# Kernel optimization log

Measured on AMD Instinct MI355X. Metric: run time of the kernel, lower is better.

Reference implementation:

```python
import jax, jax.numpy as jnp
import numpy as np

BN_EPS = 1e-5

def _bn(h, gamma, beta, mean, var):
    # inference-mode BatchNorm1d
    return (h - mean) * jax.lax.rsqrt(var + BN_EPS) * gamma + beta


def setup_inputs() -> dict:
    key = jax.random.key(0)
    ks = jax.random.split(key, 16)
    N, E, D_in, D, L = 100000, 640000, 256, 128, 3
    s = 0.05
    return {
        "x": jax.random.normal(ks[0], (N, D_in), jnp.float32),
        "edge_index": jax.random.randint(ks[1], (2, E), 0, N, jnp.int32),
        "W_in": jax.random.normal(ks[2], (D_in, D), jnp.float32) * s,
        "b_in": jax.random.normal(ks[3], (D,), jnp.float32) * s,
        "bn_in_gamma": jax.random.uniform(ks[4], (D,), jnp.float32, 0.5, 1.5),
        "bn_in_beta": jax.random.normal(ks[5], (D,), jnp.float32) * s,
        "bn_in_mean": jax.random.normal(ks[6], (D,), jnp.float32) * s,
        "bn_in_var": jax.random.uniform(ks[7], (D,), jnp.float32, 0.5, 1.5),
        "Wl": jax.random.normal(ks[8], (L, D, D), jnp.float32) * s,
        "bl": jax.random.normal(ks[9], (L, D), jnp.float32) * s,
        "Wr": jax.random.normal(ks[10], (L, D, D), jnp.float32) * s,
        "bn_gamma": jax.random.uniform(ks[11], (L, D), jnp.float32, 0.5, 1.5),
        "bn_beta": jax.random.normal(ks[12], (L, D), jnp.float32) * s,
        "bn_mean": jax.random.normal(ks[13], (L, D), jnp.float32) * s,
        "bn_var": jax.random.uniform(ks[14], (L, D), jnp.float32, 0.5, 1.5),
    }


def reference(x, edge_index, W_in, b_in, bn_in_gamma, bn_in_beta, bn_in_mean,
              bn_in_var, Wl, bl, Wr, bn_gamma, bn_beta, bn_mean, bn_var):
    N = x.shape[0]
    src, dst = edge_index[0], edge_index[1]
    # in-degree (clamped to 1 so isolated nodes aggregate to 0, matching PyG mean)
    deg = jax.ops.segment_sum(jnp.ones_like(dst, jnp.float32), dst, num_segments=N)
    deg = jnp.maximum(deg, 1.0)[:, None]  # [N, 1]

    # input projection + BN + ReLU (dropout = identity in eval)
    h = jax.nn.relu(_bn(x @ W_in + b_in, bn_in_gamma, bn_in_beta, bn_in_mean, bn_in_var))

    L = Wl.shape[0]
    for l in range(L):
        # SAGEConv(mean): lin_l(mean_j h_j) + lin_r(h_i)
        agg = jax.ops.segment_sum(h[src], dst, num_segments=N) / deg  # [N, D]
        h_new = agg @ Wl[l] + bl[l] + h @ Wr[l]
        h_new = jax.nn.relu(_bn(h_new, bn_gamma[l], bn_beta[l], bn_mean[l], bn_var[l]))
        h = h + h_new  # residual
    return h
```

## Files before the change

### kernel.cpp

```cpp
#include <hip/hip_runtime.h>

#define BN_EPS 1e-5f

typedef __bf16 bf16x8 __attribute__((ext_vector_type(8)));
typedef float f32x4 __attribute__((ext_vector_type(4)));
typedef unsigned int uint;
typedef unsigned short ushort;

__device__ __forceinline__ ushort f2bf(float f) {
  union { float f; uint u; } v; v.f = f;
  uint r = v.u + 0x7FFF + ((v.u >> 16) & 1);
  return (ushort)(r >> 16);
}
__device__ __forceinline__ float bf2f_lo(uint u) {
  union { uint i; float f; } v; v.i = u << 16; return v.f;
}
__device__ __forceinline__ float bf2f_hi(uint u) {
  union { uint i; float f; } v; v.i = u & 0xffff0000u; return v.f;
}
__device__ __forceinline__ uint pack2(float a, float b) {
  return (uint)f2bf(a) | ((uint)f2bf(b) << 16);
}


__global__ void hist_kernel(const int* __restrict__ dst, int* __restrict__ cnt, int E) {
  int e = blockIdx.x * 256 + threadIdx.x;
  if (e < E) atomicAdd(&cnt[dst[e]], 1);
}

__device__ __forceinline__ int block_exscan256(int v, int tid, int* ws4) {
  __syncthreads();
  int lane = tid & 63, w = tid >> 6;
  int x = v;
  #pragma unroll
  for (int off = 1; off < 64; off <<= 1) {
    int y = __shfl_up(x, off, 64);
    if (lane >= off) x += y;
  }
  if (lane == 63) ws4[w] = x;
  __syncthreads();
  if (tid == 0) {
    int s = 0;
    for (int i = 0; i < 4; ++i) { int t = ws4[i]; ws4[i] = s; s += t; }
  }
  __syncthreads();
  return ws4[w] + x - v;
}

__global__ void blocksum_kernel(const int* __restrict__ cnt, int* __restrict__ bsum, int N) {
  __shared__ int ws4[4];
  int tid = threadIdx.x;
  int i = blockIdx.x * 256 + tid;
  int v = (i < N) ? cnt[i] : 0;
  #pragma unroll
  for (int off = 32; off > 0; off >>= 1) v += __shfl_down(v, off, 64);
  if ((tid & 63) == 0) ws4[tid >> 6] = v;
  __syncthreads();
  if (tid == 0) bsum[blockIdx.x] = ws4[0] + ws4[1] + ws4[2] + ws4[3];
}

__global__ void scanbsum_kernel(const int* __restrict__ bsum, int* __restrict__ boff,
                                int NB, int* __restrict__ rowptr, int N, int E) {
  __shared__ int ws4[4];
  __shared__ int tot;
  int tid = threadIdx.x;
  int carry = 0;
  for (int base = 0; base < NB; base += 256) {
    int i = base + tid;
    int v = (i < NB) ? bsum[i] : 0;
    int ex = block_exscan256(v, tid, ws4);
    if (i < NB) boff[i] = carry + ex;
    if (tid == 255) tot = ex + v;
    __syncthreads();
    carry += tot;
  }
  if (tid == 0) rowptr[N] = E;
}

__global__ void writerowptr_kernel(const int* __restrict__ cnt, const int* __restrict__ boff,
                                   int* __restrict__ rowptr, int N) {
  __shared__ int ws4[4];
  int tid = threadIdx.x;
  int i = blockIdx.x * 256 + tid;
  int v = (i < N) ? cnt[i] : 0;
  int ex = block_exscan256(v, tid, ws4);
  if (i < N) rowptr[i] = boff[blockIdx.x] + ex;
}

__global__ void fill_kernel(const int* __restrict__ src, const int* __restrict__ dst,
                            const int* __restrict__ rowptr, int* __restrict__ cur,
                            int* __restrict__ col, int E) {
  int e = blockIdx.x * 256 + threadIdx.x;
  if (e < E) {
    int d = dst[e];
    int p = rowptr[d] + atomicAdd(&cur[d], 1);
    col[p] = src[e];
  }
}


__global__ void prep_weights_fm(const float* __restrict__ W_in, const float* __restrict__ Wl,
                                const float* __restrict__ Wr, ushort* __restrict__ Bfm) {
  int p = blockIdx.x * 256 + threadIdx.x;
  int mat = p >> 12;
  int rem = p & 4095;
  int half = rem >> 11;
  int rem2 = rem & 2047;
  int nt = rem2 >> 8, kt2 = (rem2 >> 6) & 3, lane = rem2 & 63;
  int n = nt * 16 + (lane & 15);
  int k0 = (half * 4 + kt2) * 32 + (lane >> 4) * 8;
  ushort tmp[8];
  #pragma unroll
  for (int j = 0; j < 8; ++j) {
    int k = k0 + j;
    float v;
    if (mat == 0) v = W_in[k * 128 + n];
    else {
      int l = mat - 1;
      v = (k < 128) ? Wl[l * 16384 + k * 128 + n] : Wr[l * 16384 + (k - 128) * 128 + n];
    }
    tmp[j] = f2bf(v);
  }
  *(uint4*)&Bfm[(size_t)p * 8] = *(const uint4*)tmp;
}


__global__ void agg_kernel(const int* __restrict__ rowptr, const int* __restrict__ col,
                           const ushort* __restrict__ h, ushort* __restrict__ agg, int N) {
  int node = blockIdx.x * 8 + (threadIdx.x >> 5);
  if (node >= N) return;
  int lane = threadIdx.x & 31;
  const ushort* hp = h + lane * 4;
  int beg = rowptr[node], end = rowptr[node + 1];
  int deg = end - beg;
  float di = 1.0f / (float)(deg > 0 ? deg : 1);
  float a0 = 0.f, a1 = 0.f, a2 = 0.f, a3 = 0.f;
  int e = beg;
  for (; e + 3 < end; e += 4) {
    uint2 v0 = *(const uint2*)(hp + (size_t)col[e] * 128);
    uint2 v1 = *(const uint2*)(hp + (size_t)col[e + 1] * 128);
    uint2 v2 = *(const uint2*)(hp + (size_t)col[e + 2] * 128);
    uint2 v3 = *(const uint2*)(hp + (size_t)col[e + 3] * 128);
    a0 += (bf2f_lo(v0.x) + bf2f_lo(v1.x)) + (bf2f_lo(v2.x) + bf2f_lo(v3.x));
    a1 += (bf2f_hi(v0.x) + bf2f_hi(v1.x)) + (bf2f_hi(v2.x) + bf2f_hi(v3.x));
    a2 += (bf2f_lo(v0.y) + bf2f_lo(v1.y)) + (bf2f_lo(v2.y) + bf2f_lo(v3.y));
    a3 += (bf2f_hi(v0.y) + bf2f_hi(v1.y)) + (bf2f_hi(v2.y) + bf2f_hi(v3.y));
  }
  for (; e < end; ++e) {
    uint2 v0 = *(const uint2*)(hp + (size_t)col[e] * 128);
    a0 += bf2f_lo(v0.x); a1 += bf2f_hi(v0.x);
    a2 += bf2f_lo(v0.y); a3 += bf2f_hi(v0.y);
  }
  uint2 o;
  o.x = pack2(a0 * di, a1 * di);
  o.y = pack2(a2 * di, a3 * di);
  *(uint2*)(agg + (size_t)node * 128 + lane * 4) = o;
}


template<bool F32OUT>
__global__ __launch_bounds__(256, 4)
void gemm_layer(const ushort* __restrict__ A0, const ushort* __restrict__ A1,
                const ushort* __restrict__ Bfm, const float* __restrict__ bias,
                const float* __restrict__ gamma, const float* __restrict__ beta,
                const float* __restrict__ mean, const float* __restrict__ var,
                const ushort* __restrict__ residual, void* __restrict__ out, int N) {
  __shared__ float Cb_all[4 * 16 * 68];
  int tid = threadIdx.x, wave = tid >> 6, lane = tid & 63;
  int wm = wave >> 1, wn = wave & 1, quad = lane >> 4, l16 = lane & 15;
  int m0 = blockIdx.x * 64;

  int rowm[2];
  #pragma unroll
  for (int mt = 0; mt < 2; ++mt) {
    int r = m0 + wm * 32 + mt * 16 + l16;
    rowm[mt] = r < N ? r : N - 1;
  }

  uint4 a_buf[2][2], b_buf[2][4];
  #pragma unroll
  for (int mt = 0; mt < 2; ++mt)
    a_buf[0][mt] = *(const uint4*)(A0 + (size_t)rowm[mt] * 128 + quad * 8);
  {
    const ushort* bp = Bfm + (size_t)(wn * 4 * 256 + lane) * 8;
    #pragma unroll
    for (int nt = 0; nt < 4; ++nt)
      b_buf[0][nt] = *(const uint4*)(bp + nt * 2048);
  }

  f32x4 acc[2][4] = {};

  #pragma unroll
  for (int kt = 0; kt < 8; ++kt) {
    if (kt < 7) {
      int k1 = kt + 1;
      const ushort* bse = (k1 < 4) ? A0 : A1;
      int ko = (k1 & 3) * 32 + quad * 8;
      #pragma unroll
      for (int mt = 0; mt < 2; ++mt)
        a_buf[k1 & 1][mt] = *(const uint4*)(bse + (size_t)rowm[mt] * 128 + ko);
      const ushort* bp = Bfm + ((size_t)(k1 >> 2) * 16384 +
                                (size_t)((wn * 4) * 256 + (k1 & 3) * 64 + lane) * 8);
      #pragma unroll
      for (int nt = 0; nt < 4; ++nt)
        b_buf[k1 & 1][nt] = *(const uint4*)(bp + nt * 2048);
    }
    __builtin_amdgcn_sched_barrier(0);
    #pragma unroll
    for (int mt = 0; mt < 2; ++mt) {
      bf16x8 af = __builtin_bit_cast(bf16x8, a_buf[kt & 1][mt]);
      #pragma unroll
      for (int nt = 0; nt < 4; ++nt)
        acc[mt][nt] = __builtin_amdgcn_mfma_f32_16x16x32_bf16(
            af, __builtin_bit_cast(bf16x8, b_buf[kt & 1][nt]), acc[mt][nt], 0, 0, 0);
    }
  }

  #pragma unroll
  for (int nt = 0; nt < 4; ++nt) {
    int c = wn * 64 + nt * 16 + l16;
    float sc = gamma[c] * rsqrtf(var[c] + BN_EPS);
    float sh = beta[c] - mean[c] * sc;
    float bi = bias[c];
    #pragma unroll
    for (int mt = 0; mt < 2; ++mt)
      #pragma unroll
      for (int r = 0; r < 4; ++r)
        acc[mt][nt][r] = fmaxf((acc[mt][nt][r] + bi) * sc + sh, 0.f);
  }

  float* Cb = Cb_all + wave * (16 * 68);
  #pragma unroll
  for (int mt = 0; mt < 2; ++mt) {
    #pragma unroll
    for (int nt = 0; nt < 4; ++nt)
      #pragma unroll
      for (int r = 0; r < 4; ++r)
        Cb[(quad * 4 + r) * 68 + nt * 16 + l16] = acc[mt][nt][r];
    #pragma unroll
    for (int i = 0; i < 4; ++i) {
      int idx = i * 64 + lane, rowl = idx >> 4, seg = idx & 15;
      int grow = m0 + wm * 32 + mt * 16 + rowl;
      if (grow < N) {
        float4 vv = *(float4*)&Cb[rowl * 68 + seg * 4];
        uint2 rv = *(const uint2*)(residual + (size_t)grow * 128 + wn * 64 + seg * 4);
        vv.x += bf2f_lo(rv.x); vv.y += bf2f_hi(rv.x);
        vv.z += bf2f_lo(rv.y); vv.w += bf2f_hi(rv.y);
        if (F32OUT) {
          *(float4*)((float*)out + (size_t)grow * 128 + wn * 64 + seg * 4) = vv;
        } else {
          uint2 o;
          o.x = pack2(vv.x, vv.y); o.y = pack2(vv.z, vv.w);
          *(uint2*)((ushort*)out + (size_t)grow * 128 + wn * 64 + seg * 4) = o;
        }
      }
    }
  }
}


__global__ __launch_bounds__(256, 4)
void gemm_in(const float* __restrict__ X, const ushort* __restrict__ Bfm,
             const float* __restrict__ bias,
             const float* __restrict__ gamma, const float* __restrict__ beta,
             const float* __restrict__ mean, const float* __restrict__ var,
             ushort* __restrict__ out, int N) {
  __shared__ float Cb_all[4 * 16 * 68];
  int tid = threadIdx.x, wave = tid >> 6, lane = tid & 63;
  int wm = wave >> 1, wn = wave & 1, quad = lane >> 4, l16 = lane & 15;
  int m0 = blockIdx.x * 64;

  int rowm[2];
  #pragma unroll
  for (int mt = 0; mt < 2; ++mt) {
    int r = m0 + wm * 32 + mt * 16 + l16;
    rowm[mt] = r < N ? r : N - 1;
  }

  float4 f_buf[2][2][2];
  uint4 b_buf[2][4];
  #pragma unroll
  for (int mt = 0; mt < 2; ++mt) {
    const float* p = X + (size_t)rowm[mt] * 256 + quad * 8;
    f_buf[0][mt][0] = *(const float4*)p;
    f_buf[0][mt][1] = *(const float4*)(p + 4);
  }
  {
    const ushort* bp = Bfm + (size_t)(wn * 4 * 256 + lane) * 8;
    #pragma unroll
    for (int nt = 0; nt < 4; ++nt)
      b_buf[0][nt] = *(const uint4*)(bp + nt * 2048);
  }

  f32x4 acc[2][4] = {};

  #pragma unroll
  for (int kt = 0; kt < 8; ++kt) {
    if (kt < 7) {
      int k1 = kt + 1;
      int ko = k1 * 32 + quad * 8;
      #pragma unroll
      for (int mt = 0; mt < 2; ++mt) {
        const float* p = X + (size_t)rowm[mt] * 256 + ko;
        f_buf[k1 & 1][mt][0] = *(const float4*)p;
        f_buf[k1 & 1][mt][1] = *(const float4*)(p + 4);
      }
      const ushort* bp = Bfm + ((size_t)(k1 >> 2) * 16384 +
                                (size_t)((wn * 4) * 256 + (k1 & 3) * 64 + lane) * 8);
      #pragma unroll
      for (int nt = 0; nt < 4; ++nt)
        b_buf[k1 & 1][nt] = *(const uint4*)(bp + nt * 2048);
    }
    __builtin_amdgcn_sched_barrier(0);
    #pragma unroll
    for (int mt = 0; mt < 2; ++mt) {
      float4 lo = f_buf[kt & 1][mt][0], hi = f_buf[kt & 1][mt][1];
      uint4 av;
      av.x = pack2(lo.x, lo.y); av.y = pack2(lo.z, lo.w);
      av.z = pack2(hi.x, hi.y); av.w = pack2(hi.z, hi.w);
      bf16x8 af = __builtin_bit_cast(bf16x8, av);
      #pragma unroll
      for (int nt = 0; nt < 4; ++nt)
        acc[mt][nt] = __builtin_amdgcn_mfma_f32_16x16x32_bf16(
            af, __builtin_bit_cast(bf16x8, b_buf[kt & 1][nt]), acc[mt][nt], 0, 0, 0);
    }
  }

  #pragma unroll
  for (int nt = 0; nt < 4; ++nt) {
    int c = wn * 64 + nt * 16 + l16;
    float sc = gamma[c] * rsqrtf(var[c] + BN_EPS);
    float sh = beta[c] - mean[c] * sc;
    float bi = bias[c];
    #pragma unroll
    for (int mt = 0; mt < 2; ++mt)
      #pragma unroll
      for (int r = 0; r < 4; ++r)
        acc[mt][nt][r] = fmaxf((acc[mt][nt][r] + bi) * sc + sh, 0.f);
  }

  float* Cb = Cb_all + wave * (16 * 68);
  #pragma unroll
  for (int mt = 0; mt < 2; ++mt) {
    #pragma unroll
    for (int nt = 0; nt < 4; ++nt)
      #pragma unroll
      for (int r = 0; r < 4; ++r)
        Cb[(quad * 4 + r) * 68 + nt * 16 + l16] = acc[mt][nt][r];
    #pragma unroll
    for (int i = 0; i < 4; ++i) {
      int idx = i * 64 + lane, rowl = idx >> 4, seg = idx & 15;
      int grow = m0 + wm * 32 + mt * 16 + rowl;
      if (grow < N) {
        float4 vv = *(float4*)&Cb[rowl * 68 + seg * 4];
        uint2 o;
        o.x = pack2(vv.x, vv.y); o.y = pack2(vv.z, vv.w);
        *(uint2*)(out + (size_t)grow * 128 + wn * 64 + seg * 4) = o;
      }
    }
  }
}


extern "C" void kernel_launch(void* const* d_in, const int* in_sizes, int n_in,
                              void* d_out, int out_size, void* d_ws, size_t ws_size,
                              hipStream_t stream) {
  const float* x      = (const float*)d_in[0];
  const int*   eidx   = (const int*)d_in[1];
  const float* W_in   = (const float*)d_in[2];
  const float* b_in   = (const float*)d_in[3];
  const float* bng_in = (const float*)d_in[4];
  const float* bnb_in = (const float*)d_in[5];
  const float* bnm_in = (const float*)d_in[6];
  const float* bnv_in = (const float*)d_in[7];
  const float* Wl     = (const float*)d_in[8];
  const float* bl     = (const float*)d_in[9];
  const float* Wr     = (const float*)d_in[10];
  const float* bng    = (const float*)d_in[11];
  const float* bnb    = (const float*)d_in[12];
  const float* bnm    = (const float*)d_in[13];
  const float* bnv    = (const float*)d_in[14];

  const int N = in_sizes[0] / 256;
  const int E = in_sizes[1] / 2;
  const int NB = (N + 255) / 256;
  const int* src = eidx;
  const int* dst = eidx + E;

  char* ws = (char*)d_ws;
  size_t off = 0;
  auto alloc = [&](size_t bytes) {
    void* p = ws + off;
    off = (off + bytes + 255) & ~(size_t)255;
    return p;
  };
  int* cnt      = (int*)alloc((size_t)N * 4);
  int* rowptr   = (int*)alloc((size_t)(N + 1) * 4);
  int* bsum     = (int*)alloc((size_t)NB * 4);
  int* boff     = (int*)alloc((size_t)NB * 4);
  int* col      = (int*)alloc((size_t)E * 4);
  ushort* Bfm   = (ushort*)alloc(4 * 32768 * 2);
  ushort* hA    = (ushort*)alloc((size_t)N * 128 * 2);
  ushort* hB    = (ushort*)alloc((size_t)N * 128 * 2);
  ushort* agg   = (ushort*)alloc((size_t)N * 128 * 2);
  (void)ws_size; (void)n_in; (void)out_size;

  const int EB = (E + 255) / 256;
  const int GB = (N + 63) / 64;

  hipMemsetAsync(cnt, 0, (size_t)N * 4, stream);
  hist_kernel<<<EB, 256, 0, stream>>>(dst, cnt, E);
  blocksum_kernel<<<NB, 256, 0, stream>>>(cnt, bsum, N);
  scanbsum_kernel<<<1, 256, 0, stream>>>(bsum, boff, NB, rowptr, N, E);
  writerowptr_kernel<<<NB, 256, 0, stream>>>(cnt, boff, rowptr, N);
  hipMemsetAsync(cnt, 0, (size_t)N * 4, stream);
  fill_kernel<<<EB, 256, 0, stream>>>(src, dst, rowptr, cnt, col, E);

  prep_weights_fm<<<64, 256, 0, stream>>>(W_in, Wl, Wr, Bfm);

  gemm_in<<<GB, 256, 0, stream>>>(x, Bfm, b_in, bng_in, bnb_in, bnm_in, bnv_in, hA, N);

  ushort* hbuf[2] = { hA, hB };
  for (int l = 0; l < 3; ++l) {
    const ushort* h_in = hbuf[l & 1];
    agg_kernel<<<(N + 7) / 8, 256, 0, stream>>>(rowptr, col, h_in, agg, N);
    const ushort* BfmL = Bfm + (size_t)(l + 1) * 32768;
    const float* biasL = bl + l * 128;
    if (l < 2) {
      gemm_layer<false><<<GB, 256, 0, stream>>>(agg, h_in, BfmL, biasL,
          bng + l * 128, bnb + l * 128, bnm + l * 128, bnv + l * 128,
          h_in, (void*)hbuf[(l + 1) & 1], N);
    } else {
      gemm_layer<true><<<GB, 256, 0, stream>>>(agg, h_in, BfmL, biasL,
          bng + l * 128, bnb + l * 128, bnm + l * 128, bnv + l * 128,
          h_in, d_out, N);
    }
  }
}
```

Measured before the change: 457.4 us.

## Fuse neighbor aggregation into layer GEMM and replace CSR scan with atomic reservation

```diff
diff --git a/kernel.cpp b/kernel.cpp
--- a/kernel.cpp
+++ b/kernel.cpp
@@ -28,147 +28,117 @@
   if (e < E) atomicAdd(&cnt[dst[e]], 1);
 }
 
-__device__ __forceinline__ int block_exscan256(int v, int tid, int* ws4) {
-  __syncthreads();
-  int lane = tid & 63, w = tid >> 6;
+__global__ void reserve_prep_kernel(const int* __restrict__ cnt, int* __restrict__ rowbeg,
+                                    int* __restrict__ cursor,
+                                    const float* __restrict__ W_in, const float* __restrict__ Wl,
+                                    const float* __restrict__ Wr, ushort* __restrict__ Bfm,
+                                    int NB, int N) {
+  int tid = threadIdx.x;
+  int b = blockIdx.x;
+  if (b >= NB) {
+    int p = (b - NB) * 256 + tid;
+    int mat = p >> 12;
+    int rem = p & 4095;
+    int half = rem >> 11;
+    int rem2 = rem & 2047;
+    int nt = rem2 >> 8, kt2 = (rem2 >> 6) & 3, lane = rem2 & 63;
+    int n = nt * 16 + (lane & 15);
+    int k0 = (half * 4 + kt2) * 32 + (lane >> 4) * 8;
+    ushort tmp[8];
+    #pragma unroll
+    for (int j = 0; j < 8; ++j) {
+      int k = k0 + j;
+      float v;
+      if (mat == 0) v = W_in[k * 128 + n];
+      else {
+        int l = mat - 1;
+        v = (k < 128) ? Wl[l * 16384 + k * 128 + n] : Wr[l * 16384 + (k - 128) * 128 + n];
+      }
+      tmp[j] = f2bf(v);
+    }
+    *(uint4*)&Bfm[(size_t)p * 8] = *(const uint4*)tmp;
+    return;
+  }
+  int i = b * 256 + tid;
+  int v = (i < N) ? cnt[i] : 0;
+  int lane = tid & 63;
   int x = v;
   #pragma unroll
   for (int off = 1; off < 64; off <<= 1) {
     int y = __shfl_up(x, off, 64);
     if (lane >= off) x += y;
   }
-  if (lane == 63) ws4[w] = x;
-  __syncthreads();
-  if (tid == 0) {
-    int s = 0;
-    for (int i = 0; i < 4; ++i) { int t = ws4[i]; ws4[i] = s; s += t; }
-  }
-  __syncthreads();
-  return ws4[w] + x - v;
-}
-
-__global__ void blocksum_kernel(const int* __restrict__ cnt, int* __restrict__ bsum, int N) {
-  __shared__ int ws4[4];
-  int tid = threadIdx.x;
-  int i = blockIdx.x * 256 + tid;
-  int v = (i < N) ? cnt[i] : 0;
-  #pragma unroll
-  for (int off = 32; off > 0; off >>= 1) v += __shfl_down(v, off, 64);
-  if ((tid & 63) == 0) ws4[tid >> 6] = v;
-  __syncthreads();
-  if (tid == 0) bsum[blockIdx.x] = ws4[0] + ws4[1] + ws4[2] + ws4[3];
-}
-
-__global__ void scanbsum_kernel(const int* __restrict__ bsum, int* __restrict__ boff,
-                                int NB, int* __restrict__ rowptr, int N, int E) {
-  __shared__ int ws4[4];
-  __shared__ int tot;
-  int tid = threadIdx.x;
-  int carry = 0;
-  for (int base = 0; base < NB; base += 256) {
-    int i = base + tid;
-    int v = (i < NB) ? bsum[i] : 0;
-    int ex = block_exscan256(v, tid, ws4);
-    if (i < NB) boff[i] = carry + ex;
-    if (tid == 255) tot = ex + v;
-    __syncthreads();
-    carry += tot;
-  }
-  if (tid == 0) rowptr[N] = E;
-}
-
-__global__ void writerowptr_kernel(const int* __restrict__ cnt, const int* __restrict__ boff,
-                                   int* __restrict__ rowptr, int N) {
-  __shared__ int ws4[4];
-  int tid = threadIdx.x;
-  int i = blockIdx.x * 256 + tid;
-  int v = (i < N) ? cnt[i] : 0;
-  int ex = block_exscan256(v, tid, ws4);
-  if (i < N) rowptr[i] = boff[blockIdx.x] + ex;
+  int ret = 0;
+  if (lane == 63) ret = atomicAdd(cursor, x);
+  int base = __shfl(ret, 63);
+  if (i < N) rowbeg[i] = base + x - v;
 }
 
 __global__ void fill_kernel(const int* __restrict__ src, const int* __restrict__ dst,
-                            const int* __restrict__ rowptr, int* __restrict__ cur,
+                            const int* __restrict__ rowbeg, int* __restrict__ cur,
                             int* __restrict__ col, int E) {
   int e = blockIdx.x * 256 + threadIdx.x;
   if (e < E) {
     int d = dst[e];
-    int p = rowptr[d] + atomicAdd(&cur[d], 1);
+    int p = rowbeg[d] + atomicAdd(&cur[d], 1);
     col[p] = src[e];
   }
-}
-
-
-__global__ void prep_weights_fm(const float* __restrict__ W_in, const float* __restrict__ Wl,
-                                const float* __restrict__ Wr, ushort* __restrict__ Bfm) {
-  int p = blockIdx.x * 256 + threadIdx.x;
-  int mat = p >> 12;
-  int rem = p & 4095;
-  int half = rem >> 11;
-  int rem2 = rem & 2047;
-  int nt = rem2 >> 8, kt2 = (rem2 >> 6) & 3, lane = rem2 & 63;
-  int n = nt * 16 + (lane & 15);
-  int k0 = (half * 4 + kt2) * 32 + (lane >> 4) * 8;
-  ushort tmp[8];
-  #pragma unroll
-  for (int j = 0; j < 8; ++j) {
-    int k = k0 + j;
-    float v;
-    if (mat == 0) v = W_in[k * 128 + n];
-    else {
-      int l = mat - 1;
-      v = (k < 128) ? Wl[l * 16384 + k * 128 + n] : Wr[l * 16384 + (k - 128) * 128 + n];
-    }
-    tmp[j] = f2bf(v);
-  }
-  *(uint4*)&Bfm[(size_t)p * 8] = *(const uint4*)tmp;
-}
-
-
-__global__ void agg_kernel(const int* __restrict__ rowptr, const int* __restrict__ col,
-                           const ushort* __restrict__ h, ushort* __restrict__ agg, int N) {
-  int node = blockIdx.x * 8 + (threadIdx.x >> 5);
-  if (node >= N) return;
-  int lane = threadIdx.x & 31;
-  const ushort* hp = h + lane * 4;
-  int beg = rowptr[node], end = rowptr[node + 1];
-  int deg = end - beg;
-  float di = 1.0f / (float)(deg > 0 ? deg : 1);
-  float a0 = 0.f, a1 = 0.f, a2 = 0.f, a3 = 0.f;
-  int e = beg;
-  for (; e + 3 < end; e += 4) {
-    uint2 v0 = *(const uint2*)(hp + (size_t)col[e] * 128);
-    uint2 v1 = *(const uint2*)(hp + (size_t)col[e + 1] * 128);
-    uint2 v2 = *(const uint2*)(hp + (size_t)col[e + 2] * 128);
-    uint2 v3 = *(const uint2*)(hp + (size_t)col[e + 3] * 128);
-    a0 += (bf2f_lo(v0.x) + bf2f_lo(v1.x)) + (bf2f_lo(v2.x) + bf2f_lo(v3.x));
-    a1 += (bf2f_hi(v0.x) + bf2f_hi(v1.x)) + (bf2f_hi(v2.x) + bf2f_hi(v3.x));
-    a2 += (bf2f_lo(v0.y) + bf2f_lo(v1.y)) + (bf2f_lo(v2.y) + bf2f_lo(v3.y));
-    a3 += (bf2f_hi(v0.y) + bf2f_hi(v1.y)) + (bf2f_hi(v2.y) + bf2f_hi(v3.y));
-  }
-  for (; e < end; ++e) {
-    uint2 v0 = *(const uint2*)(hp + (size_t)col[e] * 128);
-    a0 += bf2f_lo(v0.x); a1 += bf2f_hi(v0.x);
-    a2 += bf2f_lo(v0.y); a3 += bf2f_hi(v0.y);
-  }
-  uint2 o;
-  o.x = pack2(a0 * di, a1 * di);
-  o.y = pack2(a2 * di, a3 * di);
-  *(uint2*)(agg + (size_t)node * 128 + lane * 4) = o;
 }
 
 
 template<bool F32OUT>
 __global__ __launch_bounds__(256, 4)
-void gemm_layer(const ushort* __restrict__ A0, const ushort* __restrict__ A1,
+void gemm_fused(const int* __restrict__ rowbeg, const int* __restrict__ deg,
+                const int* __restrict__ col, const ushort* __restrict__ h,
                 const ushort* __restrict__ Bfm, const float* __restrict__ bias,
                 const float* __restrict__ gamma, const float* __restrict__ beta,
                 const float* __restrict__ mean, const float* __restrict__ var,
-                const ushort* __restrict__ residual, void* __restrict__ out, int N) {
+                void* __restrict__ out, int N) {
+  __shared__ __align__(16) ushort Atile[64 * 128];
   __shared__ float Cb_all[4 * 16 * 68];
-  int tid = threadIdx.x, wave = tid >> 6, lane = tid & 63;
+  int tid = threadIdx.x;
+  int m0 = blockIdx.x * 64;
+
+  {
+    int hw = tid >> 5, l32 = tid & 31;
+    const ushort* hp = h + l32 * 4;
+    #pragma unroll 1
+    for (int i = 0; i < 8; ++i) {
+      int r = hw * 8 + i;
+      int node = m0 + r;
+      if (node < N) {
+        int beg = rowbeg[node];
+        int d = deg[node];
+        float di = 1.0f / (float)(d > 0 ? d : 1);
+        float a0 = 0.f, a1 = 0.f, a2 = 0.f, a3 = 0.f;
+        int e = beg, end = beg + d;
+        for (; e + 3 < end; e += 4) {
+          uint2 v0 = *(const uint2*)(hp + (size_t)col[e] * 128);
+          uint2 v1 = *(const uint2*)(hp + (size_t)col[e + 1] * 128);
+          uint2 v2 = *(const uint2*)(hp + (size_t)col[e + 2] * 128);
+          uint2 v3 = *(const uint2*)(hp + (size_t)col[e + 3] * 128);
+          a0 += (bf2f_lo(v0.x) + bf2f_lo(v1.x)) + (bf2f_lo(v2.x) + bf2f_lo(v3.x));
+          a1 += (bf2f_hi(v0.x) + bf2f_hi(v1.x)) + (bf2f_hi(v2.x) + bf2f_hi(v3.x));
+          a2 += (bf2f_lo(v0.y) + bf2f_lo(v1.y)) + (bf2f_lo(v2.y) + bf2f_lo(v3.y));
+          a3 += (bf2f_hi(v0.y) + bf2f_hi(v1.y)) + (bf2f_hi(v2.y) + bf2f_hi(v3.y));
+        }
+        for (; e < end; ++e) {
+          uint2 v0 = *(const uint2*)(hp + (size_t)col[e] * 128);
+          a0 += bf2f_lo(v0.x); a1 += bf2f_hi(v0.x);
+          a2 += bf2f_lo(v0.y); a3 += bf2f_hi(v0.y);
+        }
+        uint2 o;
+        o.x = pack2(a0 * di, a1 * di);
+        o.y = pack2(a2 * di, a3 * di);
+        int widx = (r * 128 + l32 * 4) ^ ((r & 7) << 3);
+        *(uint2*)&Atile[widx] = o;
+      }
+    }
+  }
+  __syncthreads();
+
+  int wave = tid >> 6, lane = tid & 63;
   int wm = wave >> 1, wn = wave & 1, quad = lane >> 4, l16 = lane & 15;
-  int m0 = blockIdx.x * 64;
 
   int rowm[2];
   #pragma unroll
@@ -179,8 +149,10 @@
 
   uint4 a_buf[2][2], b_buf[2][4];
   #pragma unroll
-  for (int mt = 0; mt < 2; ++mt)
-    a_buf[0][mt] = *(const uint4*)(A0 + (size_t)rowm[mt] * 128 + quad * 8);
+  for (int mt = 0; mt < 2; ++mt) {
+    int lr = wm * 32 + mt * 16 + l16;
+    a_buf[0][mt] = *(const uint4*)&Atile[(lr * 128 + quad * 8) ^ ((lr & 7) << 3)];
+  }
   {
     const ushort* bp = Bfm + (size_t)(wn * 4 * 256 + lane) * 8;
     #pragma unroll
@@ -194,11 +166,19 @@
   for (int kt = 0; kt < 8; ++kt) {
     if (kt < 7) {
       int k1 = kt + 1;
-      const ushort* bse = (k1 < 4) ? A0 : A1;
-      int ko = (k1 & 3) * 32 + quad * 8;
-      #pragma unroll
-      for (int mt = 0; mt < 2; ++mt)
-        a_buf[k1 & 1][mt] = *(const uint4*)(bse + (size_t)rowm[mt] * 128 + ko);
+      if (k1 < 4) {
+        int c = k1 * 32 + quad * 8;
+        #pragma unroll
+        for (int mt = 0; mt < 2; ++mt) {
+          int lr = wm * 32 + mt * 16 + l16;
+          a_buf[k1 & 1][mt] = *(const uint4*)&Atile[(lr * 128 + c) ^ ((lr & 7) << 3)];
+        }
+      } else {
+        int ko = (k1 & 3) * 32 + quad * 8;
+        #pragma unroll
+        for (int mt = 0; mt < 2; ++mt)
+          a_buf[k1 & 1][mt] = *(const uint4*)(h + (size_t)rowm[mt] * 128 + ko);
+      }
       const ushort* bp = Bfm + ((size_t)(k1 >> 2) * 16384 +
                                 (size_t)((wn * 4) * 256 + (k1 & 3) * 64 + lane) * 8);
       #pragma unroll
@@ -243,7 +223,7 @@
       int grow = m0 + wm * 32 + mt * 16 + rowl;
       if (grow < N) {
         float4 vv = *(float4*)&Cb[rowl * 68 + seg * 4];
-        uint2 rv = *(const uint2*)(residual + (size_t)grow * 128 + wn * 64 + seg * 4);
+        uint2 rv = *(const uint2*)(h + (size_t)grow * 128 + wn * 64 + seg * 4);
         vv.x += bf2f_lo(rv.x); vv.y += bf2f_hi(rv.x);
         vv.z += bf2f_lo(rv.y); vv.w += bf2f_hi(rv.y);
         if (F32OUT) {
@@ -394,46 +374,41 @@
     off = (off + bytes + 255) & ~(size_t)255;
     return p;
   };
-  int* cnt      = (int*)alloc((size_t)N * 4);
-  int* rowptr   = (int*)alloc((size_t)(N + 1) * 4);
-  int* bsum     = (int*)alloc((size_t)NB * 4);
-  int* boff     = (int*)alloc((size_t)NB * 4);
+  int* zreg     = (int*)alloc((size_t)(2 * N + 1) * 4);
+  int* cnt      = zreg;
+  int* cur      = zreg + N;
+  int* cursor   = zreg + 2 * N;
+  int* rowbeg   = (int*)alloc((size_t)N * 4);
   int* col      = (int*)alloc((size_t)E * 4);
   ushort* Bfm   = (ushort*)alloc(4 * 32768 * 2);
   ushort* hA    = (ushort*)alloc((size_t)N * 128 * 2);
   ushort* hB    = (ushort*)alloc((size_t)N * 128 * 2);
-  ushort* agg   = (ushort*)alloc((size_t)N * 128 * 2);
   (void)ws_size; (void)n_in; (void)out_size;
 
   const int EB = (E + 255) / 256;
   const int GB = (N + 63) / 64;
 
-  hipMemsetAsync(cnt, 0, (size_t)N * 4, stream);
+  hipMemsetAsync(zreg, 0, (size_t)(2 * N + 1) * 4, stream);
   hist_kernel<<<EB, 256, 0, stream>>>(dst, cnt, E);
-  blocksum_kernel<<<NB, 256, 0, stream>>>(cnt, bsum, N);
-  scanbsum_kernel<<<1, 256, 0, stream>>>(bsum, boff, NB, rowptr, N, E);
-  writerowptr_kernel<<<NB, 256, 0, stream>>>(cnt, boff, rowptr, N);
-  hipMemsetAsync(cnt, 0, (size_t)N * 4, stream);
-  fill_kernel<<<EB, 256, 0, stream>>>(src, dst, rowptr, cnt, col, E);
-
-  prep_weights_fm<<<64, 256, 0, stream>>>(W_in, Wl, Wr, Bfm);
+  reserve_prep_kernel<<<NB + 64, 256, 0, stream>>>(cnt, rowbeg, cursor,
+                                                   W_in, Wl, Wr, Bfm, NB, N);
+  fill_kernel<<<EB, 256, 0, stream>>>(src, dst, rowbeg, cur, col, E);
 
   gemm_in<<<GB, 256, 0, stream>>>(x, Bfm, b_in, bng_in, bnb_in, bnm_in, bnv_in, hA, N);
 
   ushort* hbuf[2] = { hA, hB };
   for (int l = 0; l < 3; ++l) {
     const ushort* h_in = hbuf[l & 1];
-    agg_kernel<<<(N + 7) / 8, 256, 0, stream>>>(rowptr, col, h_in, agg, N);
     const ushort* BfmL = Bfm + (size_t)(l + 1) * 32768;
     const float* biasL = bl + l * 128;
     if (l < 2) {
-      gemm_layer<false><<<GB, 256, 0, stream>>>(agg, h_in, BfmL, biasL,
+      gemm_fused<false><<<GB, 256, 0, stream>>>(rowbeg, cnt, col, h_in, BfmL, biasL,
           bng + l * 128, bnb + l * 128, bnm + l * 128, bnv + l * 128,
-          h_in, (void*)hbuf[(l + 1) & 1], N);
+          (void*)hbuf[(l + 1) & 1], N);
     } else {
-      gemm_layer<true><<<GB, 256, 0, stream>>>(agg, h_in, BfmL, biasL,
+      gemm_fused<true><<<GB, 256, 0, stream>>>(rowbeg, cnt, col, h_in, BfmL, biasL,
           bng + l * 128, bnb + l * 128, bnm + l * 128, bnv + l * 128,
-          h_in, d_out, N);
-    }
-  }
-}
+          d_out, N);
+    }
+  }
+}
```

Result: slower. 513.0 us (+12.2%).
